# Kernel tuning notes

Measured on AMD Instinct MI355X. Metric: run time of the kernel, lower is better.

Reference implementation:

```python
import jax, jax.numpy as jnp
import numpy as np

HEAD = 16

def setup_inputs() -> dict:
    key = jax.random.key(0)
    k1, k2, k3 = jax.random.split(key, 3)
    B, S, D = 2, 2048, 1024
    x = jax.random.normal(k1, (B, S, D), dtype=jnp.float32)
    w_qkv = jax.random.normal(k2, (D, 3 * D), dtype=jnp.float32) * (1.0 / np.sqrt(D))
    b_qkv = jnp.zeros((3 * D,), dtype=jnp.float32)
    w_out = jax.random.normal(k3, (D, D), dtype=jnp.float32) * (1.0 / np.sqrt(D))
    b_out = jnp.zeros((D,), dtype=jnp.float32)
    return {"x": x, "w_qkv": w_qkv, "b_qkv": b_qkv, "w_out": w_out, "b_out": b_out}


def reference(x, w_qkv, b_qkv, w_out, b_out):
    B, S, D = x.shape
    hd = D // HEAD  # head dim
    qkv = x @ w_qkv + b_qkv                      # [B,S,3D]
    qkv = qkv.reshape(B, S, 3, HEAD, hd)
    qkv = jnp.transpose(qkv, (2, 0, 3, 1, 4))    # [3,B,H,S,hd]
    q, k, v = qkv[0], qkv[1], qkv[2]
    scores = jnp.einsum('bhqd,bhkd->bhqk', q, k)  # [B,H,S,S]
    causal = jnp.triu(jnp.ones((S, S), dtype=bool), k=1)
    scores = jnp.where(causal, -jnp.inf, scores)
    scores = scores / jnp.sqrt(jnp.asarray(hd, dtype=x.dtype))
    attn = jax.nn.softmax(scores, axis=-1)
    z = jnp.einsum('bhqk,bhkd->bhqd', attn, v)   # [B,H,S,hd]
    z = jnp.transpose(z, (0, 2, 1, 3)).reshape(B, S, D)
    out = z @ w_out + b_out
    return out
```

## Files before the change

kernel.cpp:

```cpp
#include <hip/hip_runtime.h>

#define S_LEN  2048
#define NH     16
#define HD     64
#define DMODEL 1024

using bf16x8 = __attribute__((ext_vector_type(8))) __bf16;
using f32x4  = __attribute__((ext_vector_type(4))) float;

__device__ __forceinline__ unsigned short f2bf(float f) {
    unsigned u = __float_as_uint(f);
    u += 0x7FFFu + ((u >> 16) & 1u);
    return (unsigned short)(u >> 16);
}
__device__ __forceinline__ unsigned pk_trunc(float lo, float hi) {
    return __builtin_amdgcn_perm(__float_as_uint(hi), __float_as_uint(lo), 0x07060302u);
}

#define GLDS16(gsrc, ldst) \
    __builtin_amdgcn_global_load_lds((__attribute__((address_space(1))) void*)(gsrc), \
                                     (__attribute__((address_space(3))) void*)(ldst), 16, 0, 0)

#define WAIT_LGKM0() __builtin_amdgcn_s_waitcnt(0xC07F)

__global__ __launch_bounds__(256) void conv_x_kernel(const float* __restrict__ x,
                                                     unsigned short* __restrict__ xb) {
    int idx = (blockIdx.x * 256 + threadIdx.x) * 4;
    float4 v = *(const float4*)(x + idx);
    ushort4 o;
    o.x = f2bf(v.x); o.y = f2bf(v.y); o.z = f2bf(v.z); o.w = f2bf(v.w);
    *(ushort4*)(xb + idx) = o;
}

__global__ __launch_bounds__(256) void transpose_conv2_kernel(
    const float* __restrict__ w_qkv, const float* __restrict__ w_out,
    unsigned short* __restrict__ wqkvT, unsigned short* __restrict__ woutT) {
    __shared__ float T[32][33];
    int bx = blockIdx.x;
    const float* in;
    unsigned short* out;
    int N;
    if (bx < 96) { in = w_qkv; out = wqkvT; N = 3072; }
    else         { bx -= 96; in = w_out; out = woutT; N = 1024; }
    int r  = threadIdx.x >> 3;
    int c4 = (threadIdx.x & 7) * 4;
    int kbase = blockIdx.y * 32, nbase = bx * 32;
    float4 v = *(const float4*)(in + (size_t)(kbase + r) * N + nbase + c4);
    T[r][c4 + 0] = v.x; T[r][c4 + 1] = v.y; T[r][c4 + 2] = v.z; T[r][c4 + 3] = v.w;
    __syncthreads();
    ushort4 o;
    o.x = f2bf(T[c4 + 0][r]); o.y = f2bf(T[c4 + 1][r]);
    o.z = f2bf(T[c4 + 2][r]); o.w = f2bf(T[c4 + 3][r]);
    *(ushort4*)(out + (size_t)(nbase + r) * 1024 + kbase + c4) = o;
}

__device__ __forceinline__ void mfma_mainloop(const unsigned short* __restrict__ A,
                                              const unsigned short* __restrict__ B,
                                              int K, int m0, int n0,
                                              unsigned short* As, unsigned short* Bs,
                                              f32x4 acc[4][4]) {
    const int lane = threadIdx.x & 63, wave = threadIdx.x >> 6;
    const int quad = lane >> 4, l15 = lane & 15;
    const int wm0 = (wave >> 1) * 64, wn0 = (wave & 1) * 64;

    for (int k0 = 0; k0 < K; k0 += 32) {
        __syncthreads();
        #pragma unroll
        for (int j = 0; j < 4; ++j) {
            int c0 = j * 256 + wave * 64;
            int c  = c0 + lane;
            if (j < 2) {
                int r = c >> 2, pc = c & 3;
                int q = pc ^ ((r >> 1) & 3);
                GLDS16(A + (size_t)(m0 + r) * K + k0 + q * 8, As + c0 * 8);
            } else {
                int cc = c - 512, cb0 = c0 - 512;
                int r = cc >> 2, pc = cc & 3;
                int q = pc ^ ((r >> 1) & 3);
                GLDS16(B + (size_t)(n0 + r) * K + k0 + q * 8, Bs + cb0 * 8);
            }
        }
        __syncthreads();

        bf16x8 af[4], bfr[4];
        #pragma unroll
        for (int mi = 0; mi < 4; ++mi) {
            int r = wm0 + mi * 16 + l15;
            int pc = quad ^ ((r >> 1) & 3);
            af[mi] = *(const bf16x8*)(As + r * 32 + pc * 8);
        }
        #pragma unroll
        for (int ni = 0; ni < 4; ++ni) {
            int r = wn0 + ni * 16 + l15;
            int pc = quad ^ ((r >> 1) & 3);
            bfr[ni] = *(const bf16x8*)(Bs + r * 32 + pc * 8);
        }
        #pragma unroll
        for (int mi = 0; mi < 4; ++mi)
            #pragma unroll
            for (int ni = 0; ni < 4; ++ni)
                acc[mi][ni] = __builtin_amdgcn_mfma_f32_16x16x32_bf16(
                    af[mi], bfr[ni], acc[mi][ni], 0, 0, 0);
    }
}

__global__ __launch_bounds__(256) void gemm_qkv_kernel(
    const unsigned short* __restrict__ xb, const unsigned short* __restrict__ wT,
    const float* __restrict__ bias,
    unsigned short* __restrict__ Qt, unsigned short* __restrict__ Kh,
    unsigned short* __restrict__ Vt) {
    __shared__ __align__(16) unsigned short Sh[8192];
    unsigned short* As = Sh;
    unsigned short* Bs = Sh + 4096;

    f32x4 acc[4][4];
    #pragma unroll
    for (int i = 0; i < 4; ++i)
        #pragma unroll
        for (int j = 0; j < 4; ++j) acc[i][j] = (f32x4){0.f, 0.f, 0.f, 0.f};

    int m0 = blockIdx.y * 128, n0 = blockIdx.x * 128;
    mfma_mainloop(xb, wT, DMODEL, m0, n0, As, Bs, acc);

    const int lane = threadIdx.x & 63, wave = threadIdx.x >> 6;
    const int quad = lane >> 4, l15 = lane & 15;
    const int wm0 = (wave >> 1) * 64, wn0 = (wave & 1) * 64;

    const int colbase = n0 + wn0;
    const int t = colbase >> 10;
    const int h = (colbase >> 6) & (NH - 1);
    const float qscale = (t == 0) ? 0.125f * 1.44269504088896f : 1.0f;
    float bv[4];
    #pragma unroll
    for (int ni = 0; ni < 4; ++ni) bv[ni] = bias[colbase + ni * 16 + l15];

    __syncthreads();
    unsigned short* Lw = Sh + wave * 1536;

    #pragma unroll
    for (int mi = 0; mi < 4; ++mi) {
        int mbase = m0 + wm0 + mi * 16;
        int b = mbase >> 11, sbase = mbase & (S_LEN - 1);
        if (t == 1) {
            #pragma unroll
            for (int ni = 0; ni < 4; ++ni)
                #pragma unroll
                for (int r = 0; r < 4; ++r)
                    Lw[(quad * 4 + r) * 72 + ni * 16 + l15] =
                        f2bf(acc[mi][ni][r] + bv[ni]);
            WAIT_LGKM0();
            int rr = lane & 15, dc = (lane >> 4) * 16;
            uint4 v0 = *(const uint4*)(Lw + rr * 72 + dc);
            uint4 v1 = *(const uint4*)(Lw + rr * 72 + dc + 8);
            unsigned short* dst =
                Kh + ((size_t)(b * NH + h) * S_LEN + sbase + rr) * HD + dc;
            *(uint4*)dst = v0;
            *(uint4*)(dst + 8) = v1;
        } else {
            #pragma unroll
            for (int ni = 0; ni < 4; ++ni)
                #pragma unroll
                for (int r = 0; r < 4; ++r)
                    Lw[(ni * 16 + l15) * 24 + quad * 4 + r] =
                        f2bf((acc[mi][ni][r] + bv[ni]) * qscale);
            WAIT_LGKM0();
            int c = lane;
            uint4 v0 = *(const uint4*)(Lw + c * 24);
            uint4 v1 = *(const uint4*)(Lw + c * 24 + 8);
            unsigned short* base = (t == 0) ? Qt : Vt;
            unsigned short* dst =
                base + ((size_t)(b * NH + h) * HD + c) * S_LEN + sbase;
            *(uint4*)dst = v0;
            *(uint4*)(dst + 8) = v1;
        }
        WAIT_LGKM0();
    }
}

__global__ __launch_bounds__(256) void gemm_out_kernel(
    const unsigned short* __restrict__ zb, const unsigned short* __restrict__ wT,
    const float* __restrict__ bias, float* __restrict__ out) {
    __shared__ __align__(16) unsigned short As[128 * 32], Bs[128 * 32];
    f32x4 acc[4][4];
    #pragma unroll
    for (int i = 0; i < 4; ++i)
        #pragma unroll
        for (int j = 0; j < 4; ++j) acc[i][j] = (f32x4){0.f, 0.f, 0.f, 0.f};

    int m0 = blockIdx.y * 128, n0 = blockIdx.x * 128;
    mfma_mainloop(zb, wT, DMODEL, m0, n0, As, Bs, acc);

    const int lane = threadIdx.x & 63, wave = threadIdx.x >> 6;
    const int quad = lane >> 4, l15 = lane & 15;
    const int wm0 = (wave >> 1) * 64, wn0 = (wave & 1) * 64;
    #pragma unroll
    for (int mi = 0; mi < 4; ++mi) {
        #pragma unroll
        for (int ni = 0; ni < 4; ++ni) {
            int col = n0 + wn0 + ni * 16 + l15;
            float bvv = bias[col];
            #pragma unroll
            for (int r = 0; r < 4; ++r)
                out[(size_t)(m0 + wm0 + mi * 16 + quad * 4 + r) * DMODEL + col] =
                    acc[mi][ni][r] + bvv;
        }
    }
}

__device__ const int g_sched[47 * 4] = {
    16,0,16,-1,
    31,0,15,0,  31,16,31,1,  30,0,15,0,  15,0,15,-1,
    30,16,30,1, 29,0,14,0,   29,15,29,1, 28,0,14,0,  14,0,14,-1,
    28,15,28,1, 27,0,13,0,   27,14,27,1, 26,0,13,0,  13,0,13,-1,
    26,14,26,1, 25,0,12,0,   25,13,25,1, 24,0,12,0,  12,0,12,-1,
    24,13,24,1, 23,0,11,0,   23,12,23,1, 22,0,11,0,  11,0,11,-1,
    22,12,22,1, 21,0,10,0,   21,11,21,1, 20,0,10,0,  10,0,10,-1,
    20,11,20,1, 19,0,9,0,    19,10,19,1, 18,0,9,0,   9,0,9,-1,
    18,10,18,1, 17,0,8,0,    17,9,17,1,  8,0,8,-1,
    7,0,7,-1, 6,0,6,-1, 5,0,5,-1, 4,0,4,-1, 3,0,3,-1, 2,0,2,-1, 1,0,1,-1, 0,0,0,-1
};

__global__ __launch_bounds__(256) void attn_mfma_kernel(
    const unsigned short* __restrict__ Qt, const unsigned short* __restrict__ Kh,
    const unsigned short* __restrict__ Vt, unsigned short* __restrict__ zb,
    float* __restrict__ Zp, float* __restrict__ lp) {
    __shared__ __align__(16) unsigned short Ks[64 * 64];
    __shared__ __align__(16) unsigned short Vs[64 * 64];
    __shared__ __align__(16) unsigned short Pl[4 * 16 * 64];

    const int lane = threadIdx.x & 63, wave = threadIdx.x >> 6;
    const int quad = lane >> 4, l15 = lane & 15;
    const int bh = blockIdx.x;
    const int qt   = g_sched[blockIdx.y * 4 + 0];
    const int klo  = g_sched[blockIdx.y * 4 + 1];
    const int khi  = g_sched[blockIdx.y * 4 + 2];
    const int part = g_sched[blockIdx.y * 4 + 3];
    const int q0 = qt * 64;
    const float M0 = 12.0f;

    bf16x8 qf0, qf1;
    {
        const unsigned short* qb = Qt + (size_t)bh * HD * S_LEN + q0 + wave * 16 + l15;
        union { bf16x8 v; unsigned short u[8]; } u0, u1;
        #pragma unroll
        for (int j = 0; j < 8; ++j) {
            u0.u[j] = qb[(quad * 8 + j) * S_LEN];
            u1.u[j] = qb[(32 + quad * 8 + j) * S_LEN];
        }
        qf0 = u0.v; qf1 = u1.v;
    }

    f32x4 Z[4];
    #pragma unroll
    for (int i = 0; i < 4; ++i) Z[i] = (f32x4){0.f, 0.f, 0.f, 0.f};
    float rsum = 0.f;

    unsigned short* pw = Pl + wave * 1024;
    const int pwrow = l15 * 64;
    const int qthr  = wave * 16 + l15 - quad * 4;

    for (int kt = klo; kt <= khi; ++kt) {
        __syncthreads();
        #pragma unroll
        for (int i = 0; i < 2; ++i) {
            int c0 = (i * 4 + wave) * 64;
            int c  = c0 + lane;
            int r = c >> 3, pc = c & 7, q = pc ^ (r & 7);
            GLDS16(Kh + ((size_t)bh * S_LEN + kt * 64 + r) * HD + q * 8, Ks + c0 * 8);
        }
        #pragma unroll
        for (int i = 0; i < 2; ++i) {
            int c0 = (i * 4 + wave) * 64;
            int c  = c0 + lane;
            int d = c >> 3, pc = c & 7, q = pc ^ (d & 7);
            GLDS16(Vt + ((size_t)bh * HD + d) * S_LEN + kt * 64 + q * 8, Vs + c0 * 8);
        }
        __syncthreads();

        const bool diag = (kt == qt);
        const int nmax = diag ? wave : 3;

        #pragma unroll
        for (int n = 0; n < 4; ++n) {
            int woff = pwrow + (((2 * n + (quad >> 1)) ^ (l15 & 7)) << 3) + (quad & 1) * 4;
            if (n <= nmax) {
                int rk = n * 16 + l15;
                int x = rk & 7;
                bf16x8 kv0 = *(const bf16x8*)(Ks + rk * 64 + ((quad    ) ^ x) * 8);
                bf16x8 kv1 = *(const bf16x8*)(Ks + rk * 64 + ((4 + quad) ^ x) * 8);
                f32x4 t4 = (f32x4){-M0, -M0, -M0, -M0};
                t4 = __builtin_amdgcn_mfma_f32_16x16x32_bf16(kv0, qf0, t4, 0, 0, 0);
                t4 = __builtin_amdgcn_mfma_f32_16x16x32_bf16(kv1, qf1, t4, 0, 0, 0);
                float p[4];
                #pragma unroll
                for (int r = 0; r < 4; ++r) {
                    p[r] = exp2f(t4[r]);
                    if (diag && (n * 16 + r) > qthr) p[r] = 0.f;
                    rsum += p[r];
                }
                uint2 pk;
                pk.x = pk_trunc(p[0], p[1]);
                pk.y = pk_trunc(p[2], p[3]);
                *(uint2*)(pw + woff) = pk;
            } else {
                *(uint2*)(pw + woff) = (uint2){0u, 0u};
            }
        }

        const int khmax = diag ? (wave >> 1) : 1;
        for (int kh = 0; kh <= khmax; ++kh) {
            bf16x8 pa = *(const bf16x8*)(pw + pwrow + ((kh * 4 + quad) ^ (l15 & 7)) * 8);
            #pragma unroll
            for (int ni = 0; ni < 4; ++ni) {
                int rd = ni * 16 + l15;
                bf16x8 vb = *(const bf16x8*)(Vs + rd * 64 + ((kh * 4 + quad) ^ (rd & 7)) * 8);
                Z[ni] = __builtin_amdgcn_mfma_f32_16x16x32_bf16(vb, pa, Z[ni], 0, 0, 0);
            }
        }
    }

    rsum += __shfl_xor(rsum, 16);
    rsum += __shfl_xor(rsum, 32);

    const int ql = wave * 16 + l15;
    if (part < 0) {
        const int b = bh >> 4, h = bh & (NH - 1);
        float inv = 1.f / rsum;
        size_t rowoff = (size_t)(b * S_LEN + q0 + ql) * DMODEL + h * HD;
        #pragma unroll
        for (int ni = 0; ni < 4; ++ni) {
            ushort4 o;
            o.x = f2bf(Z[ni][0] * inv);
            o.y = f2bf(Z[ni][1] * inv);
            o.z = f2bf(Z[ni][2] * inv);
            o.w = f2bf(Z[ni][3] * inv);
            *(ushort4*)(zb + rowoff + ni * 16 + quad * 4) = o;
        }
    } else {
        const int slot = (qt - 17) * 2 + part;
        float* zpo = Zp + ((size_t)(slot * 32 + bh) * 64) * 64;
        #pragma unroll
        for (int ni = 0; ni < 4; ++ni) {
            float4 st;
            st.x = Z[ni][0]; st.y = Z[ni][1]; st.z = Z[ni][2]; st.w = Z[ni][3];
            *(float4*)(zpo + (size_t)ql * 64 + ni * 16 + quad * 4) = st;
        }
        if (quad == 0)
            lp[(size_t)(slot * 32 + bh) * 64 + ql] = rsum;
    }
}

__global__ __launch_bounds__(256) void attn_merge_kernel(
    const float* __restrict__ Zp, const float* __restrict__ lp,
    unsigned short* __restrict__ zb) {
    const int bh = blockIdx.x, qi = blockIdx.y, qt = 17 + qi;
    const int t = threadIdx.x;
    const int q = t >> 2;
    const int d0 = (t & 3) << 4;
    const int s0 = qi * 2, s1 = s0 + 1;
    float l = lp[(size_t)(s0 * 32 + bh) * 64 + q] +
              lp[(size_t)(s1 * 32 + bh) * 64 + q];
    float inv = 1.f / l;
    const float* z0 = Zp + ((size_t)(s0 * 32 + bh) * 64 + q) * 64 + d0;
    const float* z1 = Zp + ((size_t)(s1 * 32 + bh) * 64 + q) * 64 + d0;
    const int b = bh >> 4, h = bh & (NH - 1);
    unsigned short* o =
        zb + (size_t)(b * S_LEN + qt * 64 + q) * DMODEL + h * HD + d0;
    #pragma unroll
    for (int i = 0; i < 16; i += 4) {
        float4 a = *(const float4*)(z0 + i);
        float4 c = *(const float4*)(z1 + i);
        ushort4 ov;
        ov.x = f2bf((a.x + c.x) * inv);
        ov.y = f2bf((a.y + c.y) * inv);
        ov.z = f2bf((a.z + c.z) * inv);
        ov.w = f2bf((a.w + c.w) * inv);
        *(ushort4*)(o + i) = ov;
    }
}

extern "C" void kernel_launch(void* const* d_in, const int* in_sizes, int n_in,
                              void* d_out, int out_size, void* d_ws, size_t ws_size,
                              hipStream_t stream)
{
    const float* x     = (const float*)d_in[0];
    const float* w_qkv = (const float*)d_in[1];
    const float* b_qkv = (const float*)d_in[2];
    const float* w_out = (const float*)d_in[3];
    const float* b_out = (const float*)d_in[4];
    float* out = (float*)d_out;

    unsigned short* wsu   = (unsigned short*)d_ws;
    unsigned short* xb    = wsu;
    unsigned short* wqkvT = xb    + (size_t)4194304;
    unsigned short* woutT = wqkvT + (size_t)3145728;
    unsigned short* Qt    = woutT + (size_t)1048576;
    unsigned short* Kh    = Qt    + (size_t)4194304;
    unsigned short* Vt    = Kh    + (size_t)4194304;
    unsigned short* zb    = Vt    + (size_t)4194304;
    float* Zp = (float*)(zb + (size_t)4194304);
    float* lp = Zp + (size_t)30 * 32 * 64 * 64;

    const int M = 2 * S_LEN;

    conv_x_kernel<<<dim3(M * DMODEL / 1024), 256, 0, stream>>>(x, xb);
    transpose_conv2_kernel<<<dim3(128, 32), 256, 0, stream>>>(
        w_qkv, w_out, wqkvT, woutT);

    gemm_qkv_kernel<<<dim3(3 * DMODEL / 128, M / 128), 256, 0, stream>>>(
        xb, wqkvT, b_qkv, Qt, Kh, Vt);

    attn_mfma_kernel<<<dim3(2 * NH, 47), 256, 0, stream>>>(Qt, Kh, Vt, zb, Zp, lp);
    attn_merge_kernel<<<dim3(2 * NH, 15), 256, 0, stream>>>(Zp, lp, zb);

    gemm_out_kernel<<<dim3(DMODEL / 128, M / 128), 256, 0, stream>>>(
        zb, woutT, b_out, out);
}
```

Before: 201.3 us.

## Fuse prep kernels, deepen GEMM K-tile to 64, merge split attention in-kernel

The x conversion and weight transpose kernels are combined into one launch, which also zeroes a flag array. The shared GEMM main loop now stages K=64 per iteration with an 8-way XOR swizzle, halving the number of barriers per K sweep at the cost of doubled LDS per block. The separate attention merge kernel is removed: the second of each pair of split-KV blocks, found with an atomic counter, does the merge after a threadfence. Together these cut two kernel launches and some barrier overhead, but add atomics and fences.

After: 372.5 us. 85.0% more time.

```diff
diff --git a/kernel.cpp b/kernel.cpp
--- a/kernel.cpp
+++ b/kernel.cpp
@@ -23,28 +23,33 @@
 
 #define WAIT_LGKM0() __builtin_amdgcn_s_waitcnt(0xC07F)
 
-__global__ __launch_bounds__(256) void conv_x_kernel(const float* __restrict__ x,
-                                                     unsigned short* __restrict__ xb) {
-    int idx = (blockIdx.x * 256 + threadIdx.x) * 4;
-    float4 v = *(const float4*)(x + idx);
-    ushort4 o;
-    o.x = f2bf(v.x); o.y = f2bf(v.y); o.z = f2bf(v.z); o.w = f2bf(v.w);
-    *(ushort4*)(xb + idx) = o;
-}
-
-__global__ __launch_bounds__(256) void transpose_conv2_kernel(
-    const float* __restrict__ w_qkv, const float* __restrict__ w_out,
-    unsigned short* __restrict__ wqkvT, unsigned short* __restrict__ woutT) {
+__global__ __launch_bounds__(256) void prep_kernel(
+    const float* __restrict__ x, const float* __restrict__ w_qkv,
+    const float* __restrict__ w_out,
+    unsigned short* __restrict__ xb, unsigned short* __restrict__ wqkvT,
+    unsigned short* __restrict__ woutT, int* __restrict__ flags) {
     __shared__ float T[32][33];
     int bx = blockIdx.x;
+    if (bx < 4096) {
+        int idx = (bx * 256 + threadIdx.x) * 4;
+        float4 v = *(const float4*)(x + idx);
+        ushort4 o;
+        o.x = f2bf(v.x); o.y = f2bf(v.y); o.z = f2bf(v.z); o.w = f2bf(v.w);
+        *(ushort4*)(xb + idx) = o;
+        if (bx == 0)
+            for (int i = threadIdx.x; i < 480; i += 256) flags[i] = 0;
+        return;
+    }
+    int tb = bx - 4096;
+    int tcol = tb & 127, krow = tb >> 7;
     const float* in;
     unsigned short* out;
-    int N;
-    if (bx < 96) { in = w_qkv; out = wqkvT; N = 3072; }
-    else         { bx -= 96; in = w_out; out = woutT; N = 1024; }
+    int N, nbx;
+    if (tcol < 96) { in = w_qkv; out = wqkvT; N = 3072; nbx = tcol; }
+    else           { in = w_out; out = woutT; N = 1024; nbx = tcol - 96; }
     int r  = threadIdx.x >> 3;
     int c4 = (threadIdx.x & 7) * 4;
-    int kbase = blockIdx.y * 32, nbase = bx * 32;
+    int kbase = krow * 32, nbase = nbx * 32;
     float4 v = *(const float4*)(in + (size_t)(kbase + r) * N + nbase + c4);
     T[r][c4 + 0] = v.x; T[r][c4 + 1] = v.y; T[r][c4 + 2] = v.z; T[r][c4 + 3] = v.w;
     __syncthreads();
@@ -54,53 +59,50 @@
     *(ushort4*)(out + (size_t)(nbase + r) * 1024 + kbase + c4) = o;
 }
 
-__device__ __forceinline__ void mfma_mainloop(const unsigned short* __restrict__ A,
-                                              const unsigned short* __restrict__ B,
-                                              int K, int m0, int n0,
-                                              unsigned short* As, unsigned short* Bs,
-                                              f32x4 acc[4][4]) {
+__device__ __forceinline__ void mfma_mainloop64(const unsigned short* __restrict__ A,
+                                                const unsigned short* __restrict__ B,
+                                                int K, int m0, int n0,
+                                                unsigned short* As, unsigned short* Bs,
+                                                f32x4 acc[4][4]) {
     const int lane = threadIdx.x & 63, wave = threadIdx.x >> 6;
     const int quad = lane >> 4, l15 = lane & 15;
     const int wm0 = (wave >> 1) * 64, wn0 = (wave & 1) * 64;
 
-    for (int k0 = 0; k0 < K; k0 += 32) {
-        __syncthreads();
-        #pragma unroll
-        for (int j = 0; j < 4; ++j) {
-            int c0 = j * 256 + wave * 64;
+    for (int k0 = 0; k0 < K; k0 += 64) {
+        __syncthreads();
+        #pragma unroll
+        for (int j = 0; j < 8; ++j) {
+            int c0 = (j & 3) * 256 + wave * 64;
             int c  = c0 + lane;
-            if (j < 2) {
-                int r = c >> 2, pc = c & 3;
-                int q = pc ^ ((r >> 1) & 3);
+            int r = c >> 3, pc = c & 7, q = pc ^ (r & 7);
+            if (j < 4)
                 GLDS16(A + (size_t)(m0 + r) * K + k0 + q * 8, As + c0 * 8);
-            } else {
-                int cc = c - 512, cb0 = c0 - 512;
-                int r = cc >> 2, pc = cc & 3;
-                int q = pc ^ ((r >> 1) & 3);
-                GLDS16(B + (size_t)(n0 + r) * K + k0 + q * 8, Bs + cb0 * 8);
-            }
-        }
-        __syncthreads();
-
-        bf16x8 af[4], bfr[4];
+            else
+                GLDS16(B + (size_t)(n0 + r) * K + k0 + q * 8, Bs + c0 * 8);
+        }
+        __syncthreads();
+
+        bf16x8 af[2][4], bfr[2][4];
         #pragma unroll
         for (int mi = 0; mi < 4; ++mi) {
-            int r = wm0 + mi * 16 + l15;
-            int pc = quad ^ ((r >> 1) & 3);
-            af[mi] = *(const bf16x8*)(As + r * 32 + pc * 8);
+            int r = wm0 + mi * 16 + l15, x = r & 7;
+            af[0][mi] = *(const bf16x8*)(As + r * 64 + ((quad    ) ^ x) * 8);
+            af[1][mi] = *(const bf16x8*)(As + r * 64 + ((4 + quad) ^ x) * 8);
         }
         #pragma unroll
         for (int ni = 0; ni < 4; ++ni) {
-            int r = wn0 + ni * 16 + l15;
-            int pc = quad ^ ((r >> 1) & 3);
-            bfr[ni] = *(const bf16x8*)(Bs + r * 32 + pc * 8);
-        }
-        #pragma unroll
-        for (int mi = 0; mi < 4; ++mi)
-            #pragma unroll
-            for (int ni = 0; ni < 4; ++ni)
-                acc[mi][ni] = __builtin_amdgcn_mfma_f32_16x16x32_bf16(
-                    af[mi], bfr[ni], acc[mi][ni], 0, 0, 0);
+            int r = wn0 + ni * 16 + l15, x = r & 7;
+            bfr[0][ni] = *(const bf16x8*)(Bs + r * 64 + ((quad    ) ^ x) * 8);
+            bfr[1][ni] = *(const bf16x8*)(Bs + r * 64 + ((4 + quad) ^ x) * 8);
+        }
+        #pragma unroll
+        for (int h = 0; h < 2; ++h)
+            #pragma unroll
+            for (int mi = 0; mi < 4; ++mi)
+                #pragma unroll
+                for (int ni = 0; ni < 4; ++ni)
+                    acc[mi][ni] = __builtin_amdgcn_mfma_f32_16x16x32_bf16(
+                        af[h][mi], bfr[h][ni], acc[mi][ni], 0, 0, 0);
     }
 }
 
@@ -109,9 +111,9 @@
     const float* __restrict__ bias,
     unsigned short* __restrict__ Qt, unsigned short* __restrict__ Kh,
     unsigned short* __restrict__ Vt) {
-    __shared__ __align__(16) unsigned short Sh[8192];
+    __shared__ __align__(16) unsigned short Sh[16384];
     unsigned short* As = Sh;
-    unsigned short* Bs = Sh + 4096;
+    unsigned short* Bs = Sh + 8192;
 
     f32x4 acc[4][4];
     #pragma unroll
@@ -120,7 +122,7 @@
         for (int j = 0; j < 4; ++j) acc[i][j] = (f32x4){0.f, 0.f, 0.f, 0.f};
 
     int m0 = blockIdx.y * 128, n0 = blockIdx.x * 128;
-    mfma_mainloop(xb, wT, DMODEL, m0, n0, As, Bs, acc);
+    mfma_mainloop64(xb, wT, DMODEL, m0, n0, As, Bs, acc);
 
     const int lane = threadIdx.x & 63, wave = threadIdx.x >> 6;
     const int quad = lane >> 4, l15 = lane & 15;
@@ -180,7 +182,7 @@
 __global__ __launch_bounds__(256) void gemm_out_kernel(
     const unsigned short* __restrict__ zb, const unsigned short* __restrict__ wT,
     const float* __restrict__ bias, float* __restrict__ out) {
-    __shared__ __align__(16) unsigned short As[128 * 32], Bs[128 * 32];
+    __shared__ __align__(16) unsigned short As[8192], Bs[8192];
     f32x4 acc[4][4];
     #pragma unroll
     for (int i = 0; i < 4; ++i)
@@ -188,7 +190,7 @@
         for (int j = 0; j < 4; ++j) acc[i][j] = (f32x4){0.f, 0.f, 0.f, 0.f};
 
     int m0 = blockIdx.y * 128, n0 = blockIdx.x * 128;
-    mfma_mainloop(zb, wT, DMODEL, m0, n0, As, Bs, acc);
+    mfma_mainloop64(zb, wT, DMODEL, m0, n0, As, Bs, acc);
 
     const int lane = threadIdx.x & 63, wave = threadIdx.x >> 6;
     const int quad = lane >> 4, l15 = lane & 15;
@@ -223,10 +225,11 @@
 __global__ __launch_bounds__(256) void attn_mfma_kernel(
     const unsigned short* __restrict__ Qt, const unsigned short* __restrict__ Kh,
     const unsigned short* __restrict__ Vt, unsigned short* __restrict__ zb,
-    float* __restrict__ Zp, float* __restrict__ lp) {
+    float* __restrict__ Zp, float* __restrict__ lp, int* __restrict__ flags) {
     __shared__ __align__(16) unsigned short Ks[64 * 64];
     __shared__ __align__(16) unsigned short Vs[64 * 64];
     __shared__ __align__(16) unsigned short Pl[4 * 16 * 64];
+    __shared__ int s_merge;
 
     const int lane = threadIdx.x & 63, wave = threadIdx.x >> 6;
     const int quad = lane >> 4, l15 = lane & 15;
@@ -323,8 +326,8 @@
     rsum += __shfl_xor(rsum, 32);
 
     const int ql = wave * 16 + l15;
+    const int b = bh >> 4, h = bh & (NH - 1);
     if (part < 0) {
-        const int b = bh >> 4, h = bh & (NH - 1);
         float inv = 1.f / rsum;
         size_t rowoff = (size_t)(b * S_LEN + q0 + ql) * DMODEL + h * HD;
         #pragma unroll
@@ -337,7 +340,8 @@
             *(ushort4*)(zb + rowoff + ni * 16 + quad * 4) = o;
         }
     } else {
-        const int slot = (qt - 17) * 2 + part;
+        const int qi = qt - 17;
+        const int slot = qi * 2 + part;
         float* zpo = Zp + ((size_t)(slot * 32 + bh) * 64) * 64;
         #pragma unroll
         for (int ni = 0; ni < 4; ++ni) {
@@ -347,35 +351,37 @@
         }
         if (quad == 0)
             lp[(size_t)(slot * 32 + bh) * 64 + ql] = rsum;
-    }
-}
-
-__global__ __launch_bounds__(256) void attn_merge_kernel(
-    const float* __restrict__ Zp, const float* __restrict__ lp,
-    unsigned short* __restrict__ zb) {
-    const int bh = blockIdx.x, qi = blockIdx.y, qt = 17 + qi;
-    const int t = threadIdx.x;
-    const int q = t >> 2;
-    const int d0 = (t & 3) << 4;
-    const int s0 = qi * 2, s1 = s0 + 1;
-    float l = lp[(size_t)(s0 * 32 + bh) * 64 + q] +
-              lp[(size_t)(s1 * 32 + bh) * 64 + q];
-    float inv = 1.f / l;
-    const float* z0 = Zp + ((size_t)(s0 * 32 + bh) * 64 + q) * 64 + d0;
-    const float* z1 = Zp + ((size_t)(s1 * 32 + bh) * 64 + q) * 64 + d0;
-    const int b = bh >> 4, h = bh & (NH - 1);
-    unsigned short* o =
-        zb + (size_t)(b * S_LEN + qt * 64 + q) * DMODEL + h * HD + d0;
-    #pragma unroll
-    for (int i = 0; i < 16; i += 4) {
-        float4 a = *(const float4*)(z0 + i);
-        float4 c = *(const float4*)(z1 + i);
-        ushort4 ov;
-        ov.x = f2bf((a.x + c.x) * inv);
-        ov.y = f2bf((a.y + c.y) * inv);
-        ov.z = f2bf((a.z + c.z) * inv);
-        ov.w = f2bf((a.w + c.w) * inv);
-        *(ushort4*)(o + i) = ov;
+
+        __threadfence();
+        __syncthreads();
+        if (threadIdx.x == 0)
+            s_merge = atomicAdd(&flags[qi * 32 + bh], 1);
+        __syncthreads();
+        if (s_merge == 1) {
+            __threadfence();
+            const int t = threadIdx.x;
+            const int q = t >> 2;
+            const int d0 = (t & 3) << 4;
+            const int s0 = qi * 2, s1 = s0 + 1;
+            float l = lp[(size_t)(s0 * 32 + bh) * 64 + q] +
+                      lp[(size_t)(s1 * 32 + bh) * 64 + q];
+            float inv = 1.f / l;
+            const float* z0 = Zp + ((size_t)(s0 * 32 + bh) * 64 + q) * 64 + d0;
+            const float* z1 = Zp + ((size_t)(s1 * 32 + bh) * 64 + q) * 64 + d0;
+            unsigned short* o =
+                zb + (size_t)(b * S_LEN + qt * 64 + q) * DMODEL + h * HD + d0;
+            #pragma unroll
+            for (int i = 0; i < 16; i += 4) {
+                float4 a = *(const float4*)(z0 + i);
+                float4 c = *(const float4*)(z1 + i);
+                ushort4 ov;
+                ov.x = f2bf((a.x + c.x) * inv);
+                ov.y = f2bf((a.y + c.y) * inv);
+                ov.z = f2bf((a.z + c.z) * inv);
+                ov.w = f2bf((a.w + c.w) * inv);
+                *(ushort4*)(o + i) = ov;
+            }
+        }
     }
 }
 
@@ -398,20 +404,18 @@
     unsigned short* Kh    = Qt    + (size_t)4194304;
     unsigned short* Vt    = Kh    + (size_t)4194304;
     unsigned short* zb    = Vt    + (size_t)4194304;
-    float* Zp = (float*)(zb + (size_t)4194304);
-    float* lp = Zp + (size_t)30 * 32 * 64 * 64;
+    float* Zp  = (float*)(zb + (size_t)4194304);
+    float* lp  = Zp + (size_t)30 * 32 * 64 * 64;
+    int*   flags = (int*)(lp + (size_t)30 * 32 * 64);
 
     const int M = 2 * S_LEN;
 
-    conv_x_kernel<<<dim3(M * DMODEL / 1024), 256, 0, stream>>>(x, xb);
-    transpose_conv2_kernel<<<dim3(128, 32), 256, 0, stream>>>(
-        w_qkv, w_out, wqkvT, woutT);
+    prep_kernel<<<dim3(8192), 256, 0, stream>>>(x, w_qkv, w_out, xb, wqkvT, woutT, flags);
 
     gemm_qkv_kernel<<<dim3(3 * DMODEL / 128, M / 128), 256, 0, stream>>>(
         xb, wqkvT, b_qkv, Qt, Kh, Vt);
 
-    attn_mfma_kernel<<<dim3(2 * NH, 47), 256, 0, stream>>>(Qt, Kh, Vt, zb, Zp, lp);
-    attn_merge_kernel<<<dim3(2 * NH, 15), 256, 0, stream>>>(Zp, lp, zb);
+    attn_mfma_kernel<<<dim3(2 * NH, 47), 256, 0, stream>>>(Qt, Kh, Vt, zb, Zp, lp, flags);
 
     gemm_out_kernel<<<dim3(DMODEL / 128, M / 128), 256, 0, stream>>>(
         zb, woutT, b_out, out);
```
